# Optimization experiments

Measured on AMD Instinct MI355X. Metric: run time of the kernel, lower is better.

Reference implementation:

```python
import jax, jax.numpy as jnp
import numpy as np


def setup_inputs() -> dict:
    key = jax.random.key(0)
    k1, k2, k3, k4 = jax.random.split(key, 4)
    B, S, E = 2, 2048, 2048
    scale = 0.02  # keep logits in a sane range
    return {
        "x": jax.random.normal(k1, (B, S, E), dtype=jnp.float32),
        "rotation_params": jax.random.normal(k2, (E, E), dtype=jnp.float32) * scale,
        "entangle_params": jax.random.normal(k3, (E, E), dtype=jnp.float32) * scale,
        "w_out": jax.random.normal(k4, (E, E), dtype=jnp.float32) * scale,
        "num_heads": 16,
    }


def reference(x, rotation_params, entangle_params, w_out, num_heads):
    # x: (B, S, E); rotation/entangle/w_out: (E, E)
    B, S, E = x.shape
    H = num_heads
    hd = E // H
    q = x @ rotation_params.T          # (B, S, E)
    k = x @ entangle_params.T          # (B, S, E)
    v = x                              # identity V projection, per source
    qh = q.reshape(B, S, H, hd)
    kh = k.reshape(B, S, H, hd)
    vh = v.reshape(B, S, H, hd)
    scores = jnp.einsum("bqhd,bkhd->bhqk", qh, kh) / np.sqrt(hd)
    # per-head bias branch from source; statically dead when E != H but kept faithful
    if entangle_params.shape[0] == H:
        scores = scores + entangle_params.reshape(H, 1, 1)
    attn = jax.nn.softmax(scores, axis=-1)  # dropout is identity at inference
    out = jnp.einsum("bhqk,bkhd->bqhd", attn, vh).reshape(B, S, E)
    return out @ w_out.T
```

## Files before the change

### kernel.cpp

```cpp
#include <hip/hip_runtime.h>

typedef __attribute__((ext_vector_type(8))) __bf16 bf16x8;
typedef __attribute__((ext_vector_type(4))) float f32x4;
typedef unsigned short u16;
typedef unsigned int u32;

__device__ __forceinline__ u16 f2bf_bits(float f) {
  __bf16 h = (__bf16)f;
  u16 r;
  __builtin_memcpy(&r, &h, 2);
  return r;
}

__device__ __forceinline__ void gload_lds16(const u16* g, u16* l) {
  __builtin_amdgcn_global_load_lds(
      (const __attribute__((address_space(1))) void*)g,
      (__attribute__((address_space(3))) void*)l, 16, 0, 0);
}

__device__ __forceinline__ bf16x8 lds_read8(const u16* base, int byteoff) {
  return *reinterpret_cast<const bf16x8*>(reinterpret_cast<const char*>(base) + byteoff);
}

__global__ void cast_bf16_kernel(const float* __restrict__ in, u16* __restrict__ out, int n4) {
  int i = blockIdx.x * blockDim.x + threadIdx.x;
  if (i >= n4) return;
  float4 v = reinterpret_cast<const float4*>(in)[i];
  ushort4 o;
  o.x = f2bf_bits(v.x); o.y = f2bf_bits(v.y);
  o.z = f2bf_bits(v.z); o.w = f2bf_bits(v.w);
  reinterpret_cast<ushort4*>(out)[i] = o;
}

__global__ void build_vt_kernel(const float* __restrict__ x, u16* __restrict__ vt, int S, int E, int H) {
  __shared__ float t[32][33];
  const int bh = blockIdx.z, b = bh / H, h = bh % H;
  const int s0 = blockIdx.x * 32, d0 = blockIdx.y * 32;
  const int tx = threadIdx.x & 31, ty = threadIdx.x >> 5;
  const float* xp = x + ((size_t)b * S) * E + (size_t)h * 128;
  #pragma unroll
  for (int r = ty; r < 32; r += 8)
    t[r][tx] = xp[(size_t)(s0 + r) * E + d0 + tx];
  __syncthreads();
  u16* vp = vt + ((size_t)bh * 128 + d0) * S + s0;
  #pragma unroll
  for (int r = ty; r < 32; r += 8)
    vp[(size_t)r * S + tx] = f2bf_bits(t[tx][r]);
}

template <bool BF16OUT>
__global__ __launch_bounds__(512, 2) void gemm3_kernel(const u16* __restrict__ A,
                                                       const u16* __restrict__ B0,
                                                       const u16* __restrict__ B1,
                                                       void* __restrict__ C0,
                                                       void* __restrict__ C1,
                                                       int K, int N, int zmask) {
  __shared__ __align__(16) u16 As[2][256 * 64];
  __shared__ __align__(16) u16 Bs[2][256 * 64];
  const int tid = threadIdx.x;
  const int wave = tid >> 6, lane = tid & 63;
  const int lr = lane & 15, lh = lane >> 4;
  const int bid = blockIdx.x;
  const int xcd = bid & 7;
  const int slot = bid >> 3;
  const int z = slot & zmask;
  const int c = zmask ? (slot >> 1) : slot;
  const int bm = (xcd >> 1) * 4 + (c >> 2);
  const int bn = (xcd & 1) * 4 + (c & 3);
  const int m0 = bm << 8, n0 = bn << 8;
  const u16* Bt = z ? B1 : B0;
  void* Cout = z ? C1 : C0;
  const int wr = wave >> 2, wc = wave & 3;

  const f32x4 zf = {0.f, 0.f, 0.f, 0.f};
  f32x4 acc[8][4];
  #pragma unroll
  for (int i = 0; i < 8; ++i)
    #pragma unroll
    for (int j = 0; j < 4; ++j) acc[i][j] = zf;

  const u16* agp[4]; const u16* bgp[4]; int ldst[4];
  #pragma unroll
  for (int i = 0; i < 4; ++i) {
    const int db = i * 8192 + tid * 16;
    const int row = db >> 7;
    const int cb = (db & 127) ^ ((row & 7) << 4);
    agp[i] = A + (size_t)(m0 + row) * K + (cb >> 1);
    bgp[i] = Bt + (size_t)(n0 + row) * K + (cb >> 1);
    ldst[i] = (i * 8192 + wave * 1024) >> 1;
  }

  const int NT = K >> 6;

  #pragma unroll
  for (int i = 0; i < 4; ++i) gload_lds16(agp[i], &As[0][ldst[i]]);
  #pragma unroll
  for (int i = 0; i < 4; ++i) gload_lds16(bgp[i], &Bs[0][ldst[i]]);
  __syncthreads();

  int cur = 0;
  for (int t = 0; t < NT; ++t) {
    if (t + 1 < NT) {
      const int k0 = (t + 1) << 6;
      #pragma unroll
      for (int i = 0; i < 4; ++i) gload_lds16(agp[i] + k0, &As[cur ^ 1][ldst[i]]);
      #pragma unroll
      for (int i = 0; i < 4; ++i) gload_lds16(bgp[i] + k0, &Bs[cur ^ 1][ldst[i]]);
    }
    bf16x8 bfr[4][2];
    #pragma unroll
    for (int j = 0; j < 4; ++j) {
      const int rowB = wc * 64 + j * 16 + lr;
      #pragma unroll
      for (int ks = 0; ks < 2; ++ks)
        bfr[j][ks] = lds_read8(Bs[cur], rowB * 128 + ((ks * 64 + lh * 16) ^ ((rowB & 7) << 4)));
    }
    __builtin_amdgcn_s_setprio(1);
    #pragma unroll
    for (int i = 0; i < 8; ++i) {
      const int rowA = wr * 128 + i * 16 + lr;
      bf16x8 af0 = lds_read8(As[cur], rowA * 128 + ((lh * 16) ^ ((rowA & 7) << 4)));
      bf16x8 af1 = lds_read8(As[cur], rowA * 128 + ((64 + lh * 16) ^ ((rowA & 7) << 4)));
      #pragma unroll
      for (int j = 0; j < 4; ++j) {
        acc[i][j] = __builtin_amdgcn_mfma_f32_16x16x32_bf16(af0, bfr[j][0], acc[i][j], 0, 0, 0);
        acc[i][j] = __builtin_amdgcn_mfma_f32_16x16x32_bf16(af1, bfr[j][1], acc[i][j], 0, 0, 0);
      }
    }
    __builtin_amdgcn_s_setprio(0);
    __syncthreads();
    cur ^= 1;
  }

  #pragma unroll
  for (int i = 0; i < 8; ++i) {
    const int row0 = m0 + wr * 128 + i * 16 + lh * 4;
    #pragma unroll
    for (int j = 0; j < 4; ++j) {
      const int col = n0 + wc * 64 + j * 16 + lr;
      #pragma unroll
      for (int r = 0; r < 4; ++r) {
        const size_t idx = (size_t)(row0 + r) * N + col;
        if (BF16OUT)
          ((u16*)Cout)[idx] = f2bf_bits(acc[i][j][r]);
        else
          ((float*)Cout)[idx] = acc[i][j][r];
      }
    }
  }
}

__global__ __launch_bounds__(256, 4) void attn_kernel(const u16* __restrict__ Q,
                                                      const u16* __restrict__ Kx,
                                                      const u16* __restrict__ Vt,
                                                      u16* __restrict__ O,
                                                      int S, int E, int H) {
  __shared__ __align__(16) u16 Ks[64 * 128];
  __shared__ __align__(16) u16 Vs[128 * 64];
  __shared__ __align__(16) u16 Pl[4][16 * 64];

  const int tid = threadIdx.x;
  const int wave = tid >> 6, lane = tid & 63;
  const int lr = lane & 15, lh = lane >> 4;
  const int qb = blockIdx.x;
  const int bh = blockIdx.y;
  const int b = bh / H, h = bh % H;
  const size_t base = ((size_t)b * S) * E + (size_t)h * 128;
  const u16* Qp = Q + base;
  const u16* Kp = Kx + base;
  const u16* Vp = Vt + (size_t)bh * 128 * S;
  u16* Op = O + base;

  const int qrow = qb * 64 + wave * 16 + lr;
  bf16x8 qf[4];
  #pragma unroll
  for (int c = 0; c < 4; ++c)
    qf[c] = *reinterpret_cast<const bf16x8*>(Qp + (size_t)qrow * E + c * 32 + lh * 8);

  const int dstb = wave * 1024 + lane * 16;
  int ksrc[4], vsrc[4];
  u16 *kdst[4], *vdst[4];
  #pragma unroll
  for (int i = 0; i < 4; ++i) {
    const int db = dstb + i * 4096;
    const int s = db >> 8;
    const int kcb = (db & 255) ^ ((s & 7) << 4);
    ksrc[i] = s * E + (kcb >> 1);
    kdst[i] = Ks + ((wave * 1024 + i * 4096) >> 1);
    const int d = db >> 7;
    const int vcb = (db & 127) ^ ((d & 7) << 4);
    vsrc[i] = d * S + (vcb >> 1);
    vdst[i] = Vs + ((wave * 1024 + i * 4096) >> 1);
  }

  const f32x4 zf = {0.f, 0.f, 0.f, 0.f};
  f32x4 oacc[8];
  #pragma unroll
  for (int n = 0; n < 8; ++n) oacc[n] = zf;
  float Lp[4] = {0.f, 0.f, 0.f, 0.f};

  const float c2 = 0.12751649736230842f;
  const int swz = (lr & 7) << 4;
  u16* pw = &Pl[wave][0];

  for (int s0 = 0; s0 < S; s0 += 64) {
    #pragma unroll
    for (int i = 0; i < 4; ++i) gload_lds16(Kp + s0 * E + ksrc[i], kdst[i]);
    #pragma unroll
    for (int i = 0; i < 4; ++i) gload_lds16(Vp + s0 + vsrc[i], vdst[i]);
    __syncthreads();

    f32x4 sg[4];
    #pragma unroll
    for (int g = 0; g < 4; ++g) sg[g] = zf;
    __builtin_amdgcn_s_setprio(1);
    #pragma unroll
    for (int c = 0; c < 4; ++c) {
      const int cb = (c * 64 + lh * 16) ^ swz;
      #pragma unroll
      for (int g = 0; g < 4; ++g) {
        bf16x8 kf = lds_read8(Ks, (g * 16 + lr) * 256 + cb);
        sg[g] = __builtin_amdgcn_mfma_f32_16x16x32_bf16(qf[c], kf, sg[g], 0, 0, 0);
      }
    }
    __builtin_amdgcn_s_setprio(0);

    float p[4][4];
    #pragma unroll
    for (int g = 0; g < 4; ++g)
      #pragma unroll
      for (int j = 0; j < 4; ++j)
        p[g][j] = __builtin_exp2f(sg[g][j] * c2);
    #pragma unroll
    for (int j = 0; j < 4; ++j)
      Lp[j] += (p[0][j] + p[1][j]) + (p[2][j] + p[3][j]);

    #pragma unroll
    for (int j = 0; j < 4; ++j) {
      const int r = lh * 4 + j;
      const int rx = (r & 7) << 4;
      #pragma unroll
      for (int g = 0; g < 4; ++g) {
        const int cbp = ((g * 16 + lr) * 2) ^ rx;
        *reinterpret_cast<u16*>(reinterpret_cast<char*>(pw) + r * 128 + cbp) = f2bf_bits(p[g][j]);
      }
    }

    #pragma unroll
    for (int ks = 0; ks < 2; ++ks) {
      const int cb = ks * 64 + lh * 16;
      bf16x8 pf = lds_read8(pw, lr * 128 + (cb ^ swz));
      __builtin_amdgcn_s_setprio(1);
      #pragma unroll
      for (int n = 0; n < 8; ++n) {
        bf16x8 vf = lds_read8(Vs, (n * 16 + lr) * 128 + (cb ^ swz));
        oacc[n] = __builtin_amdgcn_mfma_f32_16x16x32_bf16(pf, vf, oacc[n], 0, 0, 0);
      }
      __builtin_amdgcn_s_setprio(0);
    }
    __syncthreads();
  }

  #pragma unroll
  for (int m = 1; m <= 8; m <<= 1)
    #pragma unroll
    for (int j = 0; j < 4; ++j)
      Lp[j] += __shfl_xor(Lp[j], m, 64);

  float inv[4];
  #pragma unroll
  for (int j = 0; j < 4; ++j) inv[j] = 1.0f / Lp[j];
  const int orow0 = qb * 64 + wave * 16 + lh * 4;
  #pragma unroll
  for (int n = 0; n < 8; ++n)
    #pragma unroll
    for (int j = 0; j < 4; ++j)
      Op[(size_t)(orow0 + j) * E + n * 16 + lr] = f2bf_bits(oacc[n][j] * inv[j]);
}

extern "C" void kernel_launch(void* const* d_in, const int* in_sizes, int n_in,
                              void* d_out, int out_size, void* d_ws, size_t ws_size,
                              hipStream_t stream) {
  const float* x    = (const float*)d_in[0];
  const float* rot  = (const float*)d_in[1];
  const float* ent  = (const float*)d_in[2];
  const float* wout = (const float*)d_in[3];
  const int B = 2, S = 2048, E = 2048, H = 16;
  const int M = B * S;
  const size_t nBSE = (size_t)M * E;
  const size_t nEE = (size_t)E * E;

  u16* xb = (u16*)d_ws;
  u16* qb = xb + nBSE;
  u16* kb = qb + nBSE;
  u16* rb = (u16*)d_out;
  u16* eb = rb + nEE;
  u16* vt = eb + nEE;
  u16* wb = kb;
  u16* ob = xb;

  cast_bf16_kernel<<<(int)(nBSE / 4 / 256), 256, 0, stream>>>(x, xb, (int)(nBSE / 4));
  cast_bf16_kernel<<<(int)(nEE / 4 / 256), 256, 0, stream>>>(rot, rb, (int)(nEE / 4));
  cast_bf16_kernel<<<(int)(nEE / 4 / 256), 256, 0, stream>>>(ent, eb, (int)(nEE / 4));

  dim3 tg(S / 32, 128 / 32, B * H);
  build_vt_kernel<<<tg, 256, 0, stream>>>(x, vt, S, E, H);

  gemm3_kernel<true><<<256, 512, 0, stream>>>(xb, rb, eb, qb, kb, E, E, 1);

  dim3 ag(S / 64, B * H);
  attn_kernel<<<ag, 256, 0, stream>>>(qb, kb, vt, ob, S, E, H);

  cast_bf16_kernel<<<(int)(nEE / 4 / 256), 256, 0, stream>>>(wout, wb, (int)(nEE / 4));

  gemm3_kernel<false><<<128, 512, 0, stream>>>(ob, wb, wb, d_out, d_out, E, E, 0);
}
```

Measured before the change: 375.9 us.

## Double-buffer attention K/V tiles and use smaller output GEMM tiles for full occupancy

The attention kernel now double-buffers K and V tiles in LDS, prefetching the next tile after a single barrier per iteration. Its blocks are remapped so heads group per XCD. The output projection GEMM uses 128-row tiles with 256 blocks so every CU gets work. Both GEMM and attention move the barrier to the loop top to drop one sync per iteration. The cost is doubled LDS per attention block, which lowers occupancy to two blocks per CU.

```diff
diff --git a/kernel.cpp b/kernel.cpp
--- a/kernel.cpp
+++ b/kernel.cpp
@@ -48,14 +48,16 @@
     vp[(size_t)r * S + tx] = f2bf_bits(t[tx][r]);
 }
 
-template <bool BF16OUT>
+template <bool BF16OUT, int BM>
 __global__ __launch_bounds__(512, 2) void gemm3_kernel(const u16* __restrict__ A,
                                                        const u16* __restrict__ B0,
                                                        const u16* __restrict__ B1,
                                                        void* __restrict__ C0,
                                                        void* __restrict__ C1,
                                                        int K, int N, int zmask) {
-  __shared__ __align__(16) u16 As[2][256 * 64];
+  constexpr int IR = BM / 32;
+  constexpr int ALD = BM / 64;
+  __shared__ __align__(16) u16 As[2][BM * 64];
   __shared__ __align__(16) u16 Bs[2][256 * 64];
   const int tid = threadIdx.x;
   const int wave = tid >> 6, lane = tid & 63;
@@ -63,29 +65,36 @@
   const int bid = blockIdx.x;
   const int xcd = bid & 7;
   const int slot = bid >> 3;
-  const int z = slot & zmask;
-  const int c = zmask ? (slot >> 1) : slot;
-  const int bm = (xcd >> 1) * 4 + (c >> 2);
-  const int bn = (xcd & 1) * 4 + (c & 3);
-  const int m0 = bm << 8, n0 = bn << 8;
+  int z, bm, bn;
+  if (BM == 256) {
+    z = slot & zmask;
+    const int c = zmask ? (slot >> 1) : slot;
+    bm = (xcd >> 1) * 4 + (c >> 2);
+    bn = (xcd & 1) * 4 + (c & 3);
+  } else {
+    z = 0;
+    bm = (xcd >> 1) * 8 + (slot >> 2);
+    bn = (xcd & 1) * 4 + (slot & 3);
+  }
+  const int m0 = bm * BM, n0 = bn << 8;
   const u16* Bt = z ? B1 : B0;
   void* Cout = z ? C1 : C0;
   const int wr = wave >> 2, wc = wave & 3;
 
   const f32x4 zf = {0.f, 0.f, 0.f, 0.f};
-  f32x4 acc[8][4];
-  #pragma unroll
-  for (int i = 0; i < 8; ++i)
+  f32x4 acc[IR][4];
+  #pragma unroll
+  for (int i = 0; i < IR; ++i)
     #pragma unroll
     for (int j = 0; j < 4; ++j) acc[i][j] = zf;
 
-  const u16* agp[4]; const u16* bgp[4]; int ldst[4];
+  const u16* agp[ALD]; const u16* bgp[4]; int ldst[4];
   #pragma unroll
   for (int i = 0; i < 4; ++i) {
     const int db = i * 8192 + tid * 16;
     const int row = db >> 7;
     const int cb = (db & 127) ^ ((row & 7) << 4);
-    agp[i] = A + (size_t)(m0 + row) * K + (cb >> 1);
+    if (i < ALD) agp[i] = A + (size_t)(m0 + row) * K + (cb >> 1);
     bgp[i] = Bt + (size_t)(n0 + row) * K + (cb >> 1);
     ldst[i] = (i * 8192 + wave * 1024) >> 1;
   }
@@ -93,17 +102,17 @@
   const int NT = K >> 6;
 
   #pragma unroll
-  for (int i = 0; i < 4; ++i) gload_lds16(agp[i], &As[0][ldst[i]]);
+  for (int i = 0; i < ALD; ++i) gload_lds16(agp[i], &As[0][ldst[i]]);
   #pragma unroll
   for (int i = 0; i < 4; ++i) gload_lds16(bgp[i], &Bs[0][ldst[i]]);
-  __syncthreads();
 
   int cur = 0;
   for (int t = 0; t < NT; ++t) {
+    __syncthreads();
     if (t + 1 < NT) {
       const int k0 = (t + 1) << 6;
       #pragma unroll
-      for (int i = 0; i < 4; ++i) gload_lds16(agp[i] + k0, &As[cur ^ 1][ldst[i]]);
+      for (int i = 0; i < ALD; ++i) gload_lds16(agp[i] + k0, &As[cur ^ 1][ldst[i]]);
       #pragma unroll
       for (int i = 0; i < 4; ++i) gload_lds16(bgp[i] + k0, &Bs[cur ^ 1][ldst[i]]);
     }
@@ -117,8 +126,8 @@
     }
     __builtin_amdgcn_s_setprio(1);
     #pragma unroll
-    for (int i = 0; i < 8; ++i) {
-      const int rowA = wr * 128 + i * 16 + lr;
+    for (int i = 0; i < IR; ++i) {
+      const int rowA = wr * (BM / 2) + i * 16 + lr;
       bf16x8 af0 = lds_read8(As[cur], rowA * 128 + ((lh * 16) ^ ((rowA & 7) << 4)));
       bf16x8 af1 = lds_read8(As[cur], rowA * 128 + ((64 + lh * 16) ^ ((rowA & 7) << 4)));
       #pragma unroll
@@ -128,13 +137,12 @@
       }
     }
     __builtin_amdgcn_s_setprio(0);
-    __syncthreads();
     cur ^= 1;
   }
 
   #pragma unroll
-  for (int i = 0; i < 8; ++i) {
-    const int row0 = m0 + wr * 128 + i * 16 + lh * 4;
+  for (int i = 0; i < IR; ++i) {
+    const int row0 = m0 + wr * (BM / 2) + i * 16 + lh * 4;
     #pragma unroll
     for (int j = 0; j < 4; ++j) {
       const int col = n0 + wc * 64 + j * 16 + lr;
@@ -150,20 +158,22 @@
   }
 }
 
-__global__ __launch_bounds__(256, 4) void attn_kernel(const u16* __restrict__ Q,
+__global__ __launch_bounds__(256, 2) void attn_kernel(const u16* __restrict__ Q,
                                                       const u16* __restrict__ Kx,
                                                       const u16* __restrict__ Vt,
                                                       u16* __restrict__ O,
                                                       int S, int E, int H) {
-  __shared__ __align__(16) u16 Ks[64 * 128];
-  __shared__ __align__(16) u16 Vs[128 * 64];
+  __shared__ __align__(16) u16 Ks[2][64 * 128];
+  __shared__ __align__(16) u16 Vs[2][128 * 64];
   __shared__ __align__(16) u16 Pl[4][16 * 64];
 
   const int tid = threadIdx.x;
   const int wave = tid >> 6, lane = tid & 63;
   const int lr = lane & 15, lh = lane >> 4;
-  const int qb = blockIdx.x;
-  const int bh = blockIdx.y;
+  const int bid = blockIdx.x;
+  const int idx = bid >> 3;
+  const int bh = (bid & 7) + 8 * (idx >> 5);
+  const int qb = idx & 31;
   const int b = bh / H, h = bh % H;
   const size_t base = ((size_t)b * S) * E + (size_t)h * 128;
   const u16* Qp = Q + base;
@@ -178,19 +188,17 @@
     qf[c] = *reinterpret_cast<const bf16x8*>(Qp + (size_t)qrow * E + c * 32 + lh * 8);
 
   const int dstb = wave * 1024 + lane * 16;
-  int ksrc[4], vsrc[4];
-  u16 *kdst[4], *vdst[4];
+  int ksrc[4], vsrc[4], ldso[4];
   #pragma unroll
   for (int i = 0; i < 4; ++i) {
     const int db = dstb + i * 4096;
     const int s = db >> 8;
     const int kcb = (db & 255) ^ ((s & 7) << 4);
     ksrc[i] = s * E + (kcb >> 1);
-    kdst[i] = Ks + ((wave * 1024 + i * 4096) >> 1);
     const int d = db >> 7;
     const int vcb = (db & 127) ^ ((d & 7) << 4);
     vsrc[i] = d * S + (vcb >> 1);
-    vdst[i] = Vs + ((wave * 1024 + i * 4096) >> 1);
+    ldso[i] = (wave * 1024 + i * 4096) >> 1;
   }
 
   const f32x4 zf = {0.f, 0.f, 0.f, 0.f};
@@ -202,13 +210,23 @@
   const float c2 = 0.12751649736230842f;
   const int swz = (lr & 7) << 4;
   u16* pw = &Pl[wave][0];
-
-  for (int s0 = 0; s0 < S; s0 += 64) {
-    #pragma unroll
-    for (int i = 0; i < 4; ++i) gload_lds16(Kp + s0 * E + ksrc[i], kdst[i]);
-    #pragma unroll
-    for (int i = 0; i < 4; ++i) gload_lds16(Vp + s0 + vsrc[i], vdst[i]);
+  const int NT = S >> 6;
+
+  #pragma unroll
+  for (int i = 0; i < 4; ++i) gload_lds16(Kp + ksrc[i], &Ks[0][ldso[i]]);
+  #pragma unroll
+  for (int i = 0; i < 4; ++i) gload_lds16(Vp + vsrc[i], &Vs[0][ldso[i]]);
+
+  int cur = 0;
+  for (int t = 0; t < NT; ++t) {
     __syncthreads();
+    if (t + 1 < NT) {
+      const int s0 = (t + 1) << 6;
+      #pragma unroll
+      for (int i = 0; i < 4; ++i) gload_lds16(Kp + s0 * E + ksrc[i], &Ks[cur ^ 1][ldso[i]]);
+      #pragma unroll
+      for (int i = 0; i < 4; ++i) gload_lds16(Vp + s0 + vsrc[i], &Vs[cur ^ 1][ldso[i]]);
+    }
 
     f32x4 sg[4];
     #pragma unroll
@@ -219,7 +237,7 @@
       const int cb = (c * 64 + lh * 16) ^ swz;
       #pragma unroll
       for (int g = 0; g < 4; ++g) {
-        bf16x8 kf = lds_read8(Ks, (g * 16 + lr) * 256 + cb);
+        bf16x8 kf = lds_read8(Ks[cur], (g * 16 + lr) * 256 + cb);
         sg[g] = __builtin_amdgcn_mfma_f32_16x16x32_bf16(qf[c], kf, sg[g], 0, 0, 0);
       }
     }
@@ -253,12 +271,12 @@
       __builtin_amdgcn_s_setprio(1);
       #pragma unroll
       for (int n = 0; n < 8; ++n) {
-        bf16x8 vf = lds_read8(Vs, (n * 16 + lr) * 128 + (cb ^ swz));
+        bf16x8 vf = lds_read8(Vs[cur], (n * 16 + lr) * 128 + (cb ^ swz));
         oacc[n] = __builtin_amdgcn_mfma_f32_16x16x32_bf16(pf, vf, oacc[n], 0, 0, 0);
       }
       __builtin_amdgcn_s_setprio(0);
     }
-    __syncthreads();
+    cur ^= 1;
   }
 
   #pragma unroll
@@ -306,12 +324,11 @@
   dim3 tg(S / 32, 128 / 32, B * H);
   build_vt_kernel<<<tg, 256, 0, stream>>>(x, vt, S, E, H);
 
-  gemm3_kernel<true><<<256, 512, 0, stream>>>(xb, rb, eb, qb, kb, E, E, 1);
-
-  dim3 ag(S / 64, B * H);
-  attn_kernel<<<ag, 256, 0, stream>>>(qb, kb, vt, ob, S, E, H);
+  gemm3_kernel<true, 256><<<256, 512, 0, stream>>>(xb, rb, eb, qb, kb, E, E, 1);
+
+  attn_kernel<<<1024, 256, 0, stream>>>(qb, kb, vt, ob, S, E, H);
 
   cast_bf16_kernel<<<(int)(nEE / 4 / 256), 256, 0, stream>>>(wout, wb, (int)(nEE / 4));
 
-  gemm3_kernel<false><<<128, 512, 0, stream>>>(ob, wb, wb, d_out, d_out, E, E, 0);
-}
+  gemm3_kernel<false, 128><<<256, 512, 0, stream>>>(ob, wb, wb, d_out, d_out, E, E, 0);
+}
```

Measured after the change: 374.4 us. Within noise of the previous version (-0.4%).
